# Optimization experiments

Hardware: AMD Instinct MI355X
Metric: run time of the kernel (lower is better)

## Reference

```python
import jax, jax.numpy as jnp
import numpy as np

N, D_IN, D_H, D_OUT, R, E, NB = 50000, 128, 128, 64, 4, 400000, 2

def _xavier(k, shape, fan_in, fan_out):
    # torch xavier_uniform with relu gain sqrt(2)
    lim = np.sqrt(2.0) * np.sqrt(6.0 / (fan_in + fan_out))
    return jax.random.uniform(k, shape, jnp.float32, -lim, lim)

def setup_inputs() -> dict:
    key = jax.random.key(0)
    ks = jax.random.split(key, 9)
    x = jax.random.normal(ks[0], (N, D_IN), dtype=jnp.float32)
    src = jax.random.randint(ks[1], (R, E), 0, N, dtype=jnp.int32)
    dst = jax.random.randint(ks[2], (R, E), 0, N, dtype=jnp.int32)
    inp = {"x": x, "src": src, "dst": dst}
    dims = [(D_IN, D_H), (D_H, D_H), (D_H, D_OUT)]
    for i, (di, do) in enumerate(dims):
        inp[f"basis{i}"] = _xavier(ks[3 + 2 * i], (NB, di, do), di, do)
        inp[f"coeff{i}"] = _xavier(ks[4 + 2 * i], (R, NB), NB, R)
    return inp

def _rel_layer(h, src, dst, basis, coeff):
    """One RelGraphConvLayer: per-relation basis weight + GraphConv(norm='both'),
    summed over relations (HeteroGraphConv aggregate='sum')."""
    n = h.shape[0]
    W = jnp.einsum('rb,bio->rio', coeff, basis)  # [R, d_in, d_out] basis-decomposed weights
    out = jnp.zeros((n, W.shape[-1]), dtype=h.dtype)
    for r in range(src.shape[0]):  # fixed small set of relations
        s, d = src[r], dst[r]
        ones = jnp.ones(s.shape[0], dtype=h.dtype)
        deg_out = jnp.maximum(jax.ops.segment_sum(ones, s, num_segments=n), 1.0)
        deg_in = jnp.maximum(jax.ops.segment_sum(ones, d, num_segments=n), 1.0)
        norm_src = deg_out ** -0.5
        norm_dst = deg_in ** -0.5
        # weight applied before aggregation (d_in >= d_out path of dgl GraphConv; math identical)
        hr = (h * norm_src[:, None]) @ W[r]            # [N, d_out]
        agg = jax.ops.segment_sum(hr[s], d, num_segments=n)  # SpMM via gather + scatter-add
        out = out + agg * norm_dst[:, None]
    return out

def reference(x, src, dst, basis0, coeff0, basis1, coeff1, basis2, coeff2):
    h = jax.nn.relu(_rel_layer(x, src, dst, basis0, coeff0))
    h = jax.nn.relu(_rel_layer(h, src, dst, basis1, coeff1))
    return _rel_layer(h, src, dst, basis2, coeff2)  # final layer: no activation
```

## Files before the change

kernel.cpp:

```cpp
#include <hip/hip_runtime.h>
#include <hip/hip_bf16.h>
#include <cstdint>
#include <cstddef>

#define NN 50000
#define RR 4
#define EE 400000
#define TE (RR*EE)
#define HR 25000
#define RN (RR*NN)
#define NSEG (NN*RR)
#define SCB2 782
#define NBK 512
#define BKSZ 98
#define CHA 4000
#define MAXSPAN 4608

using frag_ab = __attribute__((ext_vector_type(8))) short;
using frag_cd = __attribute__((ext_vector_type(4))) float;

static __device__ __forceinline__ unsigned short f2bf(float f) {
    union { float f; unsigned u; } v; v.f = f;
    unsigned r = (v.u + 0x7FFF + ((v.u >> 16) & 1)) >> 16;
    return (unsigned short)r;
}
static __device__ __forceinline__ unsigned pack2(float lo, float hi) {
    return (unsigned)f2bf(lo) | ((unsigned)f2bf(hi) << 16);
}
static __device__ __forceinline__ float blo(unsigned u) { return __uint_as_float(u << 16); }
static __device__ __forceinline__ float bhi(unsigned u) { return __uint_as_float(u & 0xFFFF0000u); }

__global__ __launch_bounds__(1024) void k_pre(const int* __restrict__ src,
                                              const int* __restrict__ dst,
                                              int* __restrict__ cnt_srcQ,
                                              int* __restrict__ cnt_dstQ,
                                              const float4* __restrict__ x4,
                                              uint2* __restrict__ o,
                                              const float* __restrict__ B0,
                                              const float* __restrict__ B1,
                                              const float* __restrict__ B2,
                                              unsigned short* __restrict__ Bt0,
                                              unsigned short* __restrict__ Bt1,
                                              unsigned short* __restrict__ Bt2) {
    __shared__ unsigned bins[HR / 2];
    int bid = blockIdx.x;
    if (bid < 64) {
        int combo = bid >> 3;
        int range = (bid >> 2) & 1;
        int qc    = bid & 3;
        int r = combo >> 1;
        int side = combo & 1;
        const int* arr = (side == 0 ? src : dst) + (size_t)r * EE + (size_t)qc * (EE / 4);
        int lo = range * HR;
        for (int i = threadIdx.x; i < HR / 2; i += 1024) bins[i] = 0;
        __syncthreads();
        const int4* a4 = (const int4*)arr;
        for (int i = threadIdx.x; i < EE / 16; i += 1024) {
            int4 v = a4[i];
            int t;
            t = v.x - lo; if ((unsigned)t < (unsigned)HR) atomicAdd(&bins[t >> 1], 1u << ((t & 1) * 16));
            t = v.y - lo; if ((unsigned)t < (unsigned)HR) atomicAdd(&bins[t >> 1], 1u << ((t & 1) * 16));
            t = v.z - lo; if ((unsigned)t < (unsigned)HR) atomicAdd(&bins[t >> 1], 1u << ((t & 1) * 16));
            t = v.w - lo; if ((unsigned)t < (unsigned)HR) atomicAdd(&bins[t >> 1], 1u << ((t & 1) * 16));
        }
        __syncthreads();
        int* outp = (side == 0 ? cnt_srcQ : cnt_dstQ) + (size_t)qc * RN + (size_t)r * NN + lo;
        for (int i = threadIdx.x; i < HR / 2; i += 1024) {
            unsigned b = bins[i];
            outp[2 * i]     = (int)(b & 0xFFFFu);
            outp[2 * i + 1] = (int)(b >> 16);
        }
    } else if (bid < 1627) {
        int i = (bid - 64) * 1024 + threadIdx.x;
        if (i < NN * 32) {
            float4 v = x4[i];
            o[i] = make_uint2(pack2(v.x, v.y), pack2(v.z, v.w));
        }
    } else {
        int t = (bid - 1627) * 1024 + threadIdx.x;
        if (t < 32768) {
            int k = t & 255, n = t >> 8;
            Bt0[t] = f2bf(B0[k * 128 + n]);
        } else if (t < 65536) {
            int i = t - 32768;
            int k = i & 255, n = i >> 8;
            Bt1[i] = f2bf(B1[k * 128 + n]);
        } else {
            int i = t - 65536;
            int k = i & 255, n = i >> 8;
            Bt2[i] = f2bf(B2[k * 64 + n]);
        }
    }
}

__global__ __launch_bounds__(256) void k_norms_partial(const int* __restrict__ cnt_srcQ,
                                                       const int* __restrict__ cnt_dstQ,
                                                       float* __restrict__ nsrc,
                                                       float* __restrict__ ndst,
                                                       int* __restrict__ cntd2,
                                                       int* __restrict__ part) {
    __shared__ int s[256];
    int t = threadIdx.x;
    int f = blockIdx.x * 256 + t;
    int v = 0;
    if (f < NSEG) {
        int d = f >> 2, r = f & 3;
        int i = r * NN + d;
        int ss = cnt_srcQ[i] + cnt_srcQ[RN + i] + cnt_srcQ[2 * RN + i] + cnt_srcQ[3 * RN + i];
        int ds = cnt_dstQ[i] + cnt_dstQ[RN + i] + cnt_dstQ[2 * RN + i] + cnt_dstQ[3 * RN + i];
        nsrc[i] = 1.0f / sqrtf(fmaxf((float)ss, 1.0f));
        ndst[i] = 1.0f / sqrtf(fmaxf((float)ds, 1.0f));
        cntd2[f] = ds;
        v = ds;
    }
    s[t] = v;
    __syncthreads();
    for (int off = 128; off > 0; off >>= 1) {
        if (t < off) s[t] += s[t + off];
        __syncthreads();
    }
    if (t == 0) part[blockIdx.x] = s[0];
}

__global__ __launch_bounds__(256) void k_emit2(const int* __restrict__ cntd2,
                                               const int* __restrict__ part,
                                               int* __restrict__ rp2,
                                               int* __restrict__ gcur) {
    __shared__ int red[256];
    __shared__ int s[256];
    int t = threadIdx.x;
    int bid = blockIdx.x;
    int acc = 0;
    for (int j = t; j < bid; j += 256) acc += part[j];
    red[t] = acc;
    __syncthreads();
    for (int off = 128; off > 0; off >>= 1) {
        if (t < off) red[t] += red[t + off];
        __syncthreads();
    }
    int offs0 = red[0];
    __syncthreads();
    int f = bid * 256 + t;
    int v = (f < NSEG) ? cntd2[f] : 0;
    s[t] = v;
    __syncthreads();
    for (int off = 1; off < 256; off <<= 1) {
        int u = (t >= off) ? s[t - off] : 0;
        __syncthreads();
        s[t] += u;
        __syncthreads();
    }
    if (f < NSEG) {
        int rv = offs0 + s[t] - v;
        rp2[f] = rv;
        if (f % (BKSZ * 4) == 0) gcur[f / (BKSZ * 4)] = rv;
    }
    if (f == NSEG - 1) {
        rp2[NSEG] = TE;
        gcur[NBK - 1] = TE;
    }
}

__global__ __launch_bounds__(256) void k_fillA(const int* __restrict__ src,
                                               const int* __restrict__ dst,
                                               int* __restrict__ gcur,
                                               unsigned* __restrict__ stage) {
    __shared__ int cnt[NBK];
    __shared__ int rcur[NBK];
    int r = blockIdx.y;
    int base_e = blockIdx.x * CHA;
    int t = threadIdx.x;
    for (int i = t; i < NBK; i += 256) cnt[i] = 0;
    __syncthreads();
    const int* dr = dst + (size_t)r * EE;
    const int* sr = src + (size_t)r * EE;
    for (int i = base_e + t; i < base_e + CHA; i += 256) {
        int d = dr[i];
        atomicAdd(&cnt[d / BKSZ], 1);
    }
    __syncthreads();
    for (int i = t; i < NBK; i += 256) rcur[i] = atomicAdd(&gcur[i], cnt[i]);
    __syncthreads();
    for (int i = base_e + t; i < base_e + CHA; i += 256) {
        int d = dr[i];
        int s = sr[i];
        int b = d / BKSZ;
        int dl = d - b * BKSZ;
        int pos = atomicAdd(&rcur[b], 1);
        stage[pos] = (unsigned)s | ((unsigned)r << 16) | ((unsigned)dl << 18);
    }
}

__global__ __launch_bounds__(256) void k_fillB(const unsigned* __restrict__ stage,
                                               const int* __restrict__ rp2,
                                               const float* __restrict__ nsrc,
                                               const float* __restrict__ ndst,
                                               uint2* __restrict__ ed) {
    __shared__ unsigned imgU[MAXSPAN];
    __shared__ float imgW[MAXSPAN];
    __shared__ int lcur[BKSZ * 4];
    __shared__ float ndL[BKSZ * 4];
    int b = blockIdx.x;
    int t = threadIdx.x;
    int node0 = b * BKSZ;
    if (node0 >= NN) return;
    int nodes = min(BKSZ, NN - node0);
    int nseg_local = nodes * 4;
    int segbase = node0 * 4;
    for (int i = t; i < nseg_local; i += 256) {
        lcur[i] = rp2[segbase + i];
        ndL[i] = ndst[(i & 3) * NN + node0 + (i >> 2)];
    }
    __syncthreads();
    int S0 = rp2[segbase];
    int S1 = rp2[segbase + nseg_local];
    int span = S1 - S0;
    if (span <= MAXSPAN) {
        for (int i = S0 + t; i < S1; i += 256) {
            unsigned w = stage[i];
            int s = (int)(w & 0xFFFFu);
            int r = (int)((w >> 16) & 3u);
            int dl = (int)(w >> 18);
            int seg = dl * 4 + r;
            int pos = atomicAdd(&lcur[seg], 1);
            int idx = pos - S0;
            imgU[idx] = w & 0x3FFFFu;
            imgW[idx] = nsrc[r * NN + s] * ndL[seg];
        }
        __syncthreads();
        for (int i = t; i < span; i += 256)
            ed[S0 + i] = make_uint2(imgU[i], __float_as_uint(imgW[i]));
    } else {
        for (int i = S0 + t; i < S1; i += 256) {
            unsigned w = stage[i];
            int s = (int)(w & 0xFFFFu);
            int r = (int)((w >> 16) & 3u);
            int dl = (int)(w >> 18);
            int seg = dl * 4 + r;
            int pos = atomicAdd(&lcur[seg], 1);
            ed[pos] = make_uint2(w & 0x3FFFFu,
                                 __float_as_uint(nsrc[r * NN + s] * ndL[seg]));
        }
    }
}

template <int BN, bool BF16OUT>
__global__ __launch_bounds__(256) void k_agg_gemm(const uint4* __restrict__ hb4,
                                                  const int* __restrict__ rp2,
                                                  const uint2* __restrict__ ed,
                                                  const float* __restrict__ coeff,
                                                  const unsigned short* __restrict__ Bt,
                                                  void* __restrict__ Cout) {
    __shared__ uint4 ldsA4[16 * 32];
    char* ldsB = (char*)ldsA4;

    int w = threadIdx.x >> 6;
    int lane = threadIdx.x & 63;
    int q = lane >> 4, hl = lane & 15;
    int node0 = blockIdx.x * 16;

    float c00 = coeff[0], c01 = coeff[1], c10 = coeff[2], c11 = coeff[3];
    float c20 = coeff[4], c21 = coeff[5], c30 = coeff[6], c31 = coeff[7];

#pragma unroll 1
    for (int k4 = 0; k4 < 4; k4++) {
        int rowl = w + k4 * 4;
        int node = node0 + rowl;
        {
            float a00 = 0.f, a01 = 0.f, a02 = 0.f, a03 = 0.f;
            float a04 = 0.f, a05 = 0.f, a06 = 0.f, a07 = 0.f;
            float a10 = 0.f, a11 = 0.f, a12 = 0.f, a13 = 0.f;
            float a14 = 0.f, a15 = 0.f, a16 = 0.f, a17 = 0.f;

            int e0 = rp2[node * 4], e1 = rp2[node * 4 + 4];
            int e = e0;
            uint2 wA = make_uint2(0u, 0u), wB = make_uint2(0u, 0u);
            if (e + 7 < e1) { wA = ed[e + q]; wB = ed[e + 4 + q]; }
            for (; e + 7 < e1; e += 8) {
                uint4 hA = hb4[(size_t)(wA.x & 0xFFFFu) * 16 + hl];
                uint4 hB = hb4[(size_t)(wB.x & 0xFFFFu) * 16 + hl];
                int eN = (e + 15 < e1) ? (e + 8) : e0;
                uint2 nA = ed[eN + q];
                uint2 nB = ed[eN + 4 + q];

                int rA = (int)(wA.x >> 16);
                int rB = (int)(wB.x >> 16);
                float wsA = __uint_as_float(wA.y);
                float wsB = __uint_as_float(wB.y);
                float wa0 = (rA == 0 ? c00 : rA == 1 ? c10 : rA == 2 ? c20 : c30) * wsA;
                float wa1 = (rA == 0 ? c01 : rA == 1 ? c11 : rA == 2 ? c21 : c31) * wsA;
                float wb0 = (rB == 0 ? c00 : rB == 1 ? c10 : rB == 2 ? c20 : c30) * wsB;
                float wb1 = (rB == 0 ? c01 : rB == 1 ? c11 : rB == 2 ? c21 : c31) * wsB;

                float h0 = blo(hA.x), h1 = bhi(hA.x), h2 = blo(hA.y), h3 = bhi(hA.y);
                float h4 = blo(hA.z), h5 = bhi(hA.z), h6 = blo(hA.w), h7 = bhi(hA.w);
                a00 += wa0 * h0; a01 += wa0 * h1; a02 += wa0 * h2; a03 += wa0 * h3;
                a04 += wa0 * h4; a05 += wa0 * h5; a06 += wa0 * h6; a07 += wa0 * h7;
                a10 += wa1 * h0; a11 += wa1 * h1; a12 += wa1 * h2; a13 += wa1 * h3;
                a14 += wa1 * h4; a15 += wa1 * h5; a16 += wa1 * h6; a17 += wa1 * h7;

                h0 = blo(hB.x); h1 = bhi(hB.x); h2 = blo(hB.y); h3 = bhi(hB.y);
                h4 = blo(hB.z); h5 = bhi(hB.z); h6 = blo(hB.w); h7 = bhi(hB.w);
                a00 += wb0 * h0; a01 += wb0 * h1; a02 += wb0 * h2; a03 += wb0 * h3;
                a04 += wb0 * h4; a05 += wb0 * h5; a06 += wb0 * h6; a07 += wb0 * h7;
                a10 += wb1 * h0; a11 += wb1 * h1; a12 += wb1 * h2; a13 += wb1 * h3;
                a14 += wb1 * h4; a15 += wb1 * h5; a16 += wb1 * h6; a17 += wb1 * h7;

                wA = nA; wB = nB;
            }
            for (; e < e1; e += 4) {
                int E = e + q;
                bool act = E < e1;
                uint2 weA = ed[act ? E : e0];
                uint4 hA = hb4[(size_t)(weA.x & 0xFFFFu) * 16 + hl];
                int rA = (int)(weA.x >> 16);
                float wsA = act ? __uint_as_float(weA.y) : 0.f;
                float wa0 = (rA == 0 ? c00 : rA == 1 ? c10 : rA == 2 ? c20 : c30) * wsA;
                float wa1 = (rA == 0 ? c01 : rA == 1 ? c11 : rA == 2 ? c21 : c31) * wsA;
                float h0 = blo(hA.x), h1 = bhi(hA.x), h2 = blo(hA.y), h3 = bhi(hA.y);
                float h4 = blo(hA.z), h5 = bhi(hA.z), h6 = blo(hA.w), h7 = bhi(hA.w);
                a00 += wa0 * h0; a01 += wa0 * h1; a02 += wa0 * h2; a03 += wa0 * h3;
                a04 += wa0 * h4; a05 += wa0 * h5; a06 += wa0 * h6; a07 += wa0 * h7;
                a10 += wa1 * h0; a11 += wa1 * h1; a12 += wa1 * h2; a13 += wa1 * h3;
                a14 += wa1 * h4; a15 += wa1 * h5; a16 += wa1 * h6; a17 += wa1 * h7;
            }

            a00 += __shfl_xor(a00, 16, 64); a00 += __shfl_xor(a00, 32, 64);
            a01 += __shfl_xor(a01, 16, 64); a01 += __shfl_xor(a01, 32, 64);
            a02 += __shfl_xor(a02, 16, 64); a02 += __shfl_xor(a02, 32, 64);
            a03 += __shfl_xor(a03, 16, 64); a03 += __shfl_xor(a03, 32, 64);
            a04 += __shfl_xor(a04, 16, 64); a04 += __shfl_xor(a04, 32, 64);
            a05 += __shfl_xor(a05, 16, 64); a05 += __shfl_xor(a05, 32, 64);
            a06 += __shfl_xor(a06, 16, 64); a06 += __shfl_xor(a06, 32, 64);
            a07 += __shfl_xor(a07, 16, 64); a07 += __shfl_xor(a07, 32, 64);
            a10 += __shfl_xor(a10, 16, 64); a10 += __shfl_xor(a10, 32, 64);
            a11 += __shfl_xor(a11, 16, 64); a11 += __shfl_xor(a11, 32, 64);
            a12 += __shfl_xor(a12, 16, 64); a12 += __shfl_xor(a12, 32, 64);
            a13 += __shfl_xor(a13, 16, 64); a13 += __shfl_xor(a13, 32, 64);
            a14 += __shfl_xor(a14, 16, 64); a14 += __shfl_xor(a14, 32, 64);
            a15 += __shfl_xor(a15, 16, 64); a15 += __shfl_xor(a15, 32, 64);
            a16 += __shfl_xor(a16, 16, 64); a16 += __shfl_xor(a16, 32, 64);
            a17 += __shfl_xor(a17, 16, 64); a17 += __shfl_xor(a17, 32, 64);

            int c = q >> 1, h4 = q & 1;
            float v0 = c ? (h4 ? a14 : a10) : (h4 ? a04 : a00);
            float v1 = c ? (h4 ? a15 : a11) : (h4 ? a05 : a01);
            float v2 = c ? (h4 ? a16 : a12) : (h4 ? a06 : a02);
            float v3 = c ? (h4 ? a17 : a13) : (h4 ? a07 : a03);
            uint2 st;
            st.x = pack2(v0, v1);
            st.y = pack2(v2, v3);
            int idx8 = c * 32 + hl * 2 + h4;
            int boff = rowl * 512 + ((idx8 * 8) ^ ((rowl & 7) << 4));
            *(uint2*)(ldsB + boff) = st;
        }
    }
    __syncthreads();

    int m = lane & 15, qq = lane >> 4;
    constexpr int NTW = BN / 64;

    frag_cd acc[NTW];
#pragma unroll
    for (int t = 0; t < NTW; t++) acc[t] = (frag_cd){0.f, 0.f, 0.f, 0.f};

    int arow = m;
#pragma unroll
    for (int kc = 0; kc < 8; kc++) {
        int aoff = arow * 512 + ((qq * 16 + kc * 64) ^ ((arow & 7) << 4));
        frag_ab a = *(const frag_ab*)(ldsB + aoff);
#pragma unroll
        for (int t = 0; t < NTW; t++) {
            int ct = w * NTW + t;
            frag_ab b = *(const frag_ab*)(Bt + (size_t)(ct * 16 + m) * 256 + kc * 32 + qq * 8);
            acc[t] = __builtin_amdgcn_mfma_f32_16x16x32_bf16(a, b, acc[t], 0, 0, 0);
        }
    }

#pragma unroll
    for (int t = 0; t < NTW; t++) {
#pragma unroll
        for (int i = 0; i < 4; i++) {
            int row = node0 + qq * 4 + i;
            int col = (w * NTW + t) * 16 + m;
            float v = acc[t][i];
            if (BF16OUT) {
                v = fmaxf(v, 0.f);
                ((unsigned short*)Cout)[(size_t)row * BN + col] = f2bf(v);
            } else {
                ((float*)Cout)[(size_t)row * BN + col] = v;
            }
        }
    }
}


extern "C" void kernel_launch(void* const* d_in, const int* in_sizes, int n_in,
                              void* d_out, int out_size, void* d_ws, size_t ws_size,
                              hipStream_t stream) {
    const float* x      = (const float*)d_in[0];
    const int*   src    = (const int*)d_in[1];
    const int*   dst    = (const int*)d_in[2];
    const float* basis0 = (const float*)d_in[3];
    const float* coeff0 = (const float*)d_in[4];
    const float* basis1 = (const float*)d_in[5];
    const float* coeff1 = (const float*)d_in[6];
    const float* basis2 = (const float*)d_in[7];
    const float* coeff2 = (const float*)d_in[8];
    float* out = (float*)d_out;

    char* p = (char*)d_ws;
    auto alloc = [&](size_t bytes) {
        char* r = p;
        p += (bytes + 255) & ~(size_t)255;
        return r;
    };
    int*   cnt_srcQ = (int*)alloc((size_t)4 * RN * 4);
    int*   cnt_dstQ = (int*)alloc((size_t)4 * RN * 4);
    float* nsrc     = (float*)alloc((size_t)RN * 4);
    float* ndst     = (float*)alloc((size_t)RN * 4);
    int*   cntd2    = (int*)alloc((size_t)NSEG * 4);
    int*   rp2      = (int*)alloc((size_t)(NSEG + 1) * 4);
    int*   part     = (int*)alloc((size_t)SCB2 * 4);
    int*   gcur     = (int*)alloc((size_t)NBK * 4);
    unsigned* stage = (unsigned*)alloc((size_t)TE * 4);
    uint2* ed       = (uint2*)alloc((size_t)TE * 8);
    unsigned* Hb    = (unsigned*)alloc((size_t)NN * 64 * 4);
    unsigned* Hb2   = (unsigned*)alloc((size_t)NN * 64 * 4);
    unsigned* Xb    = (unsigned*)alloc((size_t)NN * 64 * 4);
    unsigned short* Bt0 = (unsigned short*)alloc((size_t)128 * 256 * 2);
    unsigned short* Bt1 = (unsigned short*)alloc((size_t)128 * 256 * 2);
    unsigned short* Bt2 = (unsigned short*)alloc((size_t)64 * 256 * 2);

    k_pre<<<1707, 1024, 0, stream>>>(src, dst, cnt_srcQ, cnt_dstQ,
                                     (const float4*)x, (uint2*)Xb,
                                     basis0, basis1, basis2, Bt0, Bt1, Bt2);
    k_norms_partial<<<SCB2, 256, 0, stream>>>(cnt_srcQ, cnt_dstQ, nsrc, ndst, cntd2, part);
    k_emit2<<<SCB2, 256, 0, stream>>>(cntd2, part, rp2, gcur);
    k_fillA<<<dim3(EE / CHA, RR), 256, 0, stream>>>(src, dst, gcur, stage);
    k_fillB<<<NBK, 256, 0, stream>>>(stage, rp2, nsrc, ndst, ed);

    int fusedBlocks = NN / 16;

    k_agg_gemm<128, true><<<fusedBlocks, 256, 0, stream>>>(
        (const uint4*)Xb, rp2, ed, coeff0, Bt0, Hb);
    k_agg_gemm<128, true><<<fusedBlocks, 256, 0, stream>>>(
        (const uint4*)Hb, rp2, ed, coeff1, Bt1, Hb2);
    k_agg_gemm<64, false><<<fusedBlocks, 256, 0, stream>>>(
        (const uint4*)Hb2, rp2, ed, coeff2, Bt2, out);
}
```

Before: 376.9 us.

## Split fused aggregate+GEMM kernel into separate aggregation and MFMA GEMM kernels

Splits the fused kernel, which aggregated 16 nodes per block into LDS and then ran the MFMA GEMM, into two kernels. The aggregation kernel assigns one wave per node and writes a bf16 [N,256] intermediate to global memory, and a separate GEMM kernel reads that intermediate. This removes the __syncthreads barrier and the per-block serial loop of four nodes per wave, so aggregation waves are scheduled freely. In exchange it adds a round trip of the intermediate through global memory and three extra launches. Buffers are also reused: the second layer's output now overwrites Hb, since aggregation finishes before the GEMM writes.

```diff
diff --git a/kernel.cpp b/kernel.cpp
--- a/kernel.cpp
+++ b/kernel.cpp
@@ -244,146 +244,138 @@
     }
 }
 
-template <int BN, bool BF16OUT>
-__global__ __launch_bounds__(256) void k_agg_gemm(const uint4* __restrict__ hb4,
-                                                  const int* __restrict__ rp2,
-                                                  const uint2* __restrict__ ed,
-                                                  const float* __restrict__ coeff,
-                                                  const unsigned short* __restrict__ Bt,
-                                                  void* __restrict__ Cout) {
-    __shared__ uint4 ldsA4[16 * 32];
-    char* ldsB = (char*)ldsA4;
-
-    int w = threadIdx.x >> 6;
+__global__ __launch_bounds__(256) void k_agg(const uint4* __restrict__ hb4,
+                                             const int* __restrict__ rp2,
+                                             const uint2* __restrict__ ed,
+                                             const float* __restrict__ coeff,
+                                             uint2* __restrict__ Mb2) {
+    int wave = (blockIdx.x * 256 + threadIdx.x) >> 6;
     int lane = threadIdx.x & 63;
+    if (wave >= NN) return;
     int q = lane >> 4, hl = lane & 15;
-    int node0 = blockIdx.x * 16;
 
     float c00 = coeff[0], c01 = coeff[1], c10 = coeff[2], c11 = coeff[3];
     float c20 = coeff[4], c21 = coeff[5], c30 = coeff[6], c31 = coeff[7];
 
-#pragma unroll 1
-    for (int k4 = 0; k4 < 4; k4++) {
-        int rowl = w + k4 * 4;
-        int node = node0 + rowl;
-        {
-            float a00 = 0.f, a01 = 0.f, a02 = 0.f, a03 = 0.f;
-            float a04 = 0.f, a05 = 0.f, a06 = 0.f, a07 = 0.f;
-            float a10 = 0.f, a11 = 0.f, a12 = 0.f, a13 = 0.f;
-            float a14 = 0.f, a15 = 0.f, a16 = 0.f, a17 = 0.f;
-
-            int e0 = rp2[node * 4], e1 = rp2[node * 4 + 4];
-            int e = e0;
-            uint2 wA = make_uint2(0u, 0u), wB = make_uint2(0u, 0u);
-            if (e + 7 < e1) { wA = ed[e + q]; wB = ed[e + 4 + q]; }
-            for (; e + 7 < e1; e += 8) {
-                uint4 hA = hb4[(size_t)(wA.x & 0xFFFFu) * 16 + hl];
-                uint4 hB = hb4[(size_t)(wB.x & 0xFFFFu) * 16 + hl];
-                int eN = (e + 15 < e1) ? (e + 8) : e0;
-                uint2 nA = ed[eN + q];
-                uint2 nB = ed[eN + 4 + q];
-
-                int rA = (int)(wA.x >> 16);
-                int rB = (int)(wB.x >> 16);
-                float wsA = __uint_as_float(wA.y);
-                float wsB = __uint_as_float(wB.y);
-                float wa0 = (rA == 0 ? c00 : rA == 1 ? c10 : rA == 2 ? c20 : c30) * wsA;
-                float wa1 = (rA == 0 ? c01 : rA == 1 ? c11 : rA == 2 ? c21 : c31) * wsA;
-                float wb0 = (rB == 0 ? c00 : rB == 1 ? c10 : rB == 2 ? c20 : c30) * wsB;
-                float wb1 = (rB == 0 ? c01 : rB == 1 ? c11 : rB == 2 ? c21 : c31) * wsB;
-
-                float h0 = blo(hA.x), h1 = bhi(hA.x), h2 = blo(hA.y), h3 = bhi(hA.y);
-                float h4 = blo(hA.z), h5 = bhi(hA.z), h6 = blo(hA.w), h7 = bhi(hA.w);
-                a00 += wa0 * h0; a01 += wa0 * h1; a02 += wa0 * h2; a03 += wa0 * h3;
-                a04 += wa0 * h4; a05 += wa0 * h5; a06 += wa0 * h6; a07 += wa0 * h7;
-                a10 += wa1 * h0; a11 += wa1 * h1; a12 += wa1 * h2; a13 += wa1 * h3;
-                a14 += wa1 * h4; a15 += wa1 * h5; a16 += wa1 * h6; a17 += wa1 * h7;
-
-                h0 = blo(hB.x); h1 = bhi(hB.x); h2 = blo(hB.y); h3 = bhi(hB.y);
-                h4 = blo(hB.z); h5 = bhi(hB.z); h6 = blo(hB.w); h7 = bhi(hB.w);
-                a00 += wb0 * h0; a01 += wb0 * h1; a02 += wb0 * h2; a03 += wb0 * h3;
-                a04 += wb0 * h4; a05 += wb0 * h5; a06 += wb0 * h6; a07 += wb0 * h7;
-                a10 += wb1 * h0; a11 += wb1 * h1; a12 += wb1 * h2; a13 += wb1 * h3;
-                a14 += wb1 * h4; a15 += wb1 * h5; a16 += wb1 * h6; a17 += wb1 * h7;
-
-                wA = nA; wB = nB;
-            }
-            for (; e < e1; e += 4) {
-                int E = e + q;
-                bool act = E < e1;
-                uint2 weA = ed[act ? E : e0];
-                uint4 hA = hb4[(size_t)(weA.x & 0xFFFFu) * 16 + hl];
-                int rA = (int)(weA.x >> 16);
-                float wsA = act ? __uint_as_float(weA.y) : 0.f;
-                float wa0 = (rA == 0 ? c00 : rA == 1 ? c10 : rA == 2 ? c20 : c30) * wsA;
-                float wa1 = (rA == 0 ? c01 : rA == 1 ? c11 : rA == 2 ? c21 : c31) * wsA;
-                float h0 = blo(hA.x), h1 = bhi(hA.x), h2 = blo(hA.y), h3 = bhi(hA.y);
-                float h4 = blo(hA.z), h5 = bhi(hA.z), h6 = blo(hA.w), h7 = bhi(hA.w);
-                a00 += wa0 * h0; a01 += wa0 * h1; a02 += wa0 * h2; a03 += wa0 * h3;
-                a04 += wa0 * h4; a05 += wa0 * h5; a06 += wa0 * h6; a07 += wa0 * h7;
-                a10 += wa1 * h0; a11 += wa1 * h1; a12 += wa1 * h2; a13 += wa1 * h3;
-                a14 += wa1 * h4; a15 += wa1 * h5; a16 += wa1 * h6; a17 += wa1 * h7;
-            }
-
-            a00 += __shfl_xor(a00, 16, 64); a00 += __shfl_xor(a00, 32, 64);
-            a01 += __shfl_xor(a01, 16, 64); a01 += __shfl_xor(a01, 32, 64);
-            a02 += __shfl_xor(a02, 16, 64); a02 += __shfl_xor(a02, 32, 64);
-            a03 += __shfl_xor(a03, 16, 64); a03 += __shfl_xor(a03, 32, 64);
-            a04 += __shfl_xor(a04, 16, 64); a04 += __shfl_xor(a04, 32, 64);
-            a05 += __shfl_xor(a05, 16, 64); a05 += __shfl_xor(a05, 32, 64);
-            a06 += __shfl_xor(a06, 16, 64); a06 += __shfl_xor(a06, 32, 64);
-            a07 += __shfl_xor(a07, 16, 64); a07 += __shfl_xor(a07, 32, 64);
-            a10 += __shfl_xor(a10, 16, 64); a10 += __shfl_xor(a10, 32, 64);
-            a11 += __shfl_xor(a11, 16, 64); a11 += __shfl_xor(a11, 32, 64);
-            a12 += __shfl_xor(a12, 16, 64); a12 += __shfl_xor(a12, 32, 64);
-            a13 += __shfl_xor(a13, 16, 64); a13 += __shfl_xor(a13, 32, 64);
-            a14 += __shfl_xor(a14, 16, 64); a14 += __shfl_xor(a14, 32, 64);
-            a15 += __shfl_xor(a15, 16, 64); a15 += __shfl_xor(a15, 32, 64);
-            a16 += __shfl_xor(a16, 16, 64); a16 += __shfl_xor(a16, 32, 64);
-            a17 += __shfl_xor(a17, 16, 64); a17 += __shfl_xor(a17, 32, 64);
-
-            int c = q >> 1, h4 = q & 1;
-            float v0 = c ? (h4 ? a14 : a10) : (h4 ? a04 : a00);
-            float v1 = c ? (h4 ? a15 : a11) : (h4 ? a05 : a01);
-            float v2 = c ? (h4 ? a16 : a12) : (h4 ? a06 : a02);
-            float v3 = c ? (h4 ? a17 : a13) : (h4 ? a07 : a03);
-            uint2 st;
-            st.x = pack2(v0, v1);
-            st.y = pack2(v2, v3);
-            int idx8 = c * 32 + hl * 2 + h4;
-            int boff = rowl * 512 + ((idx8 * 8) ^ ((rowl & 7) << 4));
-            *(uint2*)(ldsB + boff) = st;
-        }
-    }
-    __syncthreads();
-
-    int m = lane & 15, qq = lane >> 4;
-    constexpr int NTW = BN / 64;
-
-    frag_cd acc[NTW];
+    float a00 = 0.f, a01 = 0.f, a02 = 0.f, a03 = 0.f;
+    float a04 = 0.f, a05 = 0.f, a06 = 0.f, a07 = 0.f;
+    float a10 = 0.f, a11 = 0.f, a12 = 0.f, a13 = 0.f;
+    float a14 = 0.f, a15 = 0.f, a16 = 0.f, a17 = 0.f;
+
+    int e0 = rp2[wave * 4], e1 = rp2[wave * 4 + 4];
+
+    int e = e0;
+    uint2 wA = make_uint2(0u, 0u), wB = make_uint2(0u, 0u);
+    if (e + 7 < e1) { wA = ed[e + q]; wB = ed[e + 4 + q]; }
+    for (; e + 7 < e1; e += 8) {
+        uint4 hA = hb4[(size_t)(wA.x & 0xFFFFu) * 16 + hl];
+        uint4 hB = hb4[(size_t)(wB.x & 0xFFFFu) * 16 + hl];
+        int eN = (e + 15 < e1) ? (e + 8) : e0;
+        uint2 nA = ed[eN + q];
+        uint2 nB = ed[eN + 4 + q];
+
+        int rA = (int)(wA.x >> 16);
+        int rB = (int)(wB.x >> 16);
+        float wsA = __uint_as_float(wA.y);
+        float wsB = __uint_as_float(wB.y);
+        float wa0 = (rA == 0 ? c00 : rA == 1 ? c10 : rA == 2 ? c20 : c30) * wsA;
+        float wa1 = (rA == 0 ? c01 : rA == 1 ? c11 : rA == 2 ? c21 : c31) * wsA;
+        float wb0 = (rB == 0 ? c00 : rB == 1 ? c10 : rB == 2 ? c20 : c30) * wsB;
+        float wb1 = (rB == 0 ? c01 : rB == 1 ? c11 : rB == 2 ? c21 : c31) * wsB;
+
+        float h0 = blo(hA.x), h1 = bhi(hA.x), h2 = blo(hA.y), h3 = bhi(hA.y);
+        float h4 = blo(hA.z), h5 = bhi(hA.z), h6 = blo(hA.w), h7 = bhi(hA.w);
+        a00 += wa0 * h0; a01 += wa0 * h1; a02 += wa0 * h2; a03 += wa0 * h3;
+        a04 += wa0 * h4; a05 += wa0 * h5; a06 += wa0 * h6; a07 += wa0 * h7;
+        a10 += wa1 * h0; a11 += wa1 * h1; a12 += wa1 * h2; a13 += wa1 * h3;
+        a14 += wa1 * h4; a15 += wa1 * h5; a16 += wa1 * h6; a17 += wa1 * h7;
+
+        h0 = blo(hB.x); h1 = bhi(hB.x); h2 = blo(hB.y); h3 = bhi(hB.y);
+        h4 = blo(hB.z); h5 = bhi(hB.z); h6 = blo(hB.w); h7 = bhi(hB.w);
+        a00 += wb0 * h0; a01 += wb0 * h1; a02 += wb0 * h2; a03 += wb0 * h3;
+        a04 += wb0 * h4; a05 += wb0 * h5; a06 += wb0 * h6; a07 += wb0 * h7;
+        a10 += wb1 * h0; a11 += wb1 * h1; a12 += wb1 * h2; a13 += wb1 * h3;
+        a14 += wb1 * h4; a15 += wb1 * h5; a16 += wb1 * h6; a17 += wb1 * h7;
+
+        wA = nA; wB = nB;
+    }
+    for (; e < e1; e += 4) {
+        int E = e + q;
+        bool act = E < e1;
+        uint2 weA = ed[act ? E : e0];
+        uint4 hA = hb4[(size_t)(weA.x & 0xFFFFu) * 16 + hl];
+        int rA = (int)(weA.x >> 16);
+        float wsA = act ? __uint_as_float(weA.y) : 0.f;
+        float wa0 = (rA == 0 ? c00 : rA == 1 ? c10 : rA == 2 ? c20 : c30) * wsA;
+        float wa1 = (rA == 0 ? c01 : rA == 1 ? c11 : rA == 2 ? c21 : c31) * wsA;
+        float h0 = blo(hA.x), h1 = bhi(hA.x), h2 = blo(hA.y), h3 = bhi(hA.y);
+        float h4 = blo(hA.z), h5 = bhi(hA.z), h6 = blo(hA.w), h7 = bhi(hA.w);
+        a00 += wa0 * h0; a01 += wa0 * h1; a02 += wa0 * h2; a03 += wa0 * h3;
+        a04 += wa0 * h4; a05 += wa0 * h5; a06 += wa0 * h6; a07 += wa0 * h7;
+        a10 += wa1 * h0; a11 += wa1 * h1; a12 += wa1 * h2; a13 += wa1 * h3;
+        a14 += wa1 * h4; a15 += wa1 * h5; a16 += wa1 * h6; a17 += wa1 * h7;
+    }
+
+    a00 += __shfl_xor(a00, 16, 64); a00 += __shfl_xor(a00, 32, 64);
+    a01 += __shfl_xor(a01, 16, 64); a01 += __shfl_xor(a01, 32, 64);
+    a02 += __shfl_xor(a02, 16, 64); a02 += __shfl_xor(a02, 32, 64);
+    a03 += __shfl_xor(a03, 16, 64); a03 += __shfl_xor(a03, 32, 64);
+    a04 += __shfl_xor(a04, 16, 64); a04 += __shfl_xor(a04, 32, 64);
+    a05 += __shfl_xor(a05, 16, 64); a05 += __shfl_xor(a05, 32, 64);
+    a06 += __shfl_xor(a06, 16, 64); a06 += __shfl_xor(a06, 32, 64);
+    a07 += __shfl_xor(a07, 16, 64); a07 += __shfl_xor(a07, 32, 64);
+    a10 += __shfl_xor(a10, 16, 64); a10 += __shfl_xor(a10, 32, 64);
+    a11 += __shfl_xor(a11, 16, 64); a11 += __shfl_xor(a11, 32, 64);
+    a12 += __shfl_xor(a12, 16, 64); a12 += __shfl_xor(a12, 32, 64);
+    a13 += __shfl_xor(a13, 16, 64); a13 += __shfl_xor(a13, 32, 64);
+    a14 += __shfl_xor(a14, 16, 64); a14 += __shfl_xor(a14, 32, 64);
+    a15 += __shfl_xor(a15, 16, 64); a15 += __shfl_xor(a15, 32, 64);
+    a16 += __shfl_xor(a16, 16, 64); a16 += __shfl_xor(a16, 32, 64);
+    a17 += __shfl_xor(a17, 16, 64); a17 += __shfl_xor(a17, 32, 64);
+
+    int c = q >> 1, h4 = q & 1;
+    float v0 = c ? (h4 ? a14 : a10) : (h4 ? a04 : a00);
+    float v1 = c ? (h4 ? a15 : a11) : (h4 ? a05 : a01);
+    float v2 = c ? (h4 ? a16 : a12) : (h4 ? a06 : a02);
+    float v3 = c ? (h4 ? a17 : a13) : (h4 ? a07 : a03);
+    uint2 st;
+    st.x = pack2(v0, v1);
+    st.y = pack2(v2, v3);
+    Mb2[(size_t)wave * 64 + c * 32 + hl * 2 + h4] = st;
+}
+
+template <int BN, bool BF16OUT>
+__global__ __launch_bounds__(256) void k_gemm(const unsigned short* __restrict__ A,
+                                              const unsigned short* __restrict__ Bt,
+                                              void* __restrict__ Cout) {
+    int wave = threadIdx.x >> 6, lane = threadIdx.x & 63;
+    int row0 = blockIdx.x * 64 + wave * 16;
+    if (row0 >= NN) return;
+    int m = lane & 15, q = lane >> 4;
+    const int NT = BN / 16;
+
+    frag_cd acc[NT];
 #pragma unroll
-    for (int t = 0; t < NTW; t++) acc[t] = (frag_cd){0.f, 0.f, 0.f, 0.f};
-
-    int arow = m;
+    for (int ct = 0; ct < NT; ct++) acc[ct] = (frag_cd){0.f, 0.f, 0.f, 0.f};
+
+    const size_t abase = (size_t)(row0 + m) * 256 + q * 8;
 #pragma unroll
     for (int kc = 0; kc < 8; kc++) {
-        int aoff = arow * 512 + ((qq * 16 + kc * 64) ^ ((arow & 7) << 4));
-        frag_ab a = *(const frag_ab*)(ldsB + aoff);
+        frag_ab a = *(const frag_ab*)(A + abase + kc * 32);
 #pragma unroll
-        for (int t = 0; t < NTW; t++) {
-            int ct = w * NTW + t;
-            frag_ab b = *(const frag_ab*)(Bt + (size_t)(ct * 16 + m) * 256 + kc * 32 + qq * 8);
-            acc[t] = __builtin_amdgcn_mfma_f32_16x16x32_bf16(a, b, acc[t], 0, 0, 0);
+        for (int ct = 0; ct < NT; ct++) {
+            frag_ab b = *(const frag_ab*)(Bt + (size_t)(ct * 16 + m) * 256 + kc * 32 + q * 8);
+            acc[ct] = __builtin_amdgcn_mfma_f32_16x16x32_bf16(a, b, acc[ct], 0, 0, 0);
         }
     }
 
 #pragma unroll
-    for (int t = 0; t < NTW; t++) {
+    for (int ct = 0; ct < NT; ct++) {
 #pragma unroll
         for (int i = 0; i < 4; i++) {
-            int row = node0 + qq * 4 + i;
-            int col = (w * NTW + t) * 16 + m;
-            float v = acc[t][i];
+            int row = row0 + q * 4 + i;
+            int col = ct * 16 + m;
+            float v = acc[ct][i];
             if (BF16OUT) {
                 v = fmaxf(v, 0.f);
                 ((unsigned short*)Cout)[(size_t)row * BN + col] = f2bf(v);
@@ -425,8 +417,8 @@
     int*   gcur     = (int*)alloc((size_t)NBK * 4);
     unsigned* stage = (unsigned*)alloc((size_t)TE * 4);
     uint2* ed       = (uint2*)alloc((size_t)TE * 8);
+    unsigned* Mb    = (unsigned*)alloc((size_t)NN * 128 * 4);
     unsigned* Hb    = (unsigned*)alloc((size_t)NN * 64 * 4);
-    unsigned* Hb2   = (unsigned*)alloc((size_t)NN * 64 * 4);
     unsigned* Xb    = (unsigned*)alloc((size_t)NN * 64 * 4);
     unsigned short* Bt0 = (unsigned short*)alloc((size_t)128 * 256 * 2);
     unsigned short* Bt1 = (unsigned short*)alloc((size_t)128 * 256 * 2);
@@ -440,12 +432,13 @@
     k_fillA<<<dim3(EE / CHA, RR), 256, 0, stream>>>(src, dst, gcur, stage);
     k_fillB<<<NBK, 256, 0, stream>>>(stage, rp2, nsrc, ndst, ed);
 
-    int fusedBlocks = NN / 16;
-
-    k_agg_gemm<128, true><<<fusedBlocks, 256, 0, stream>>>(
-        (const uint4*)Xb, rp2, ed, coeff0, Bt0, Hb);
-    k_agg_gemm<128, true><<<fusedBlocks, 256, 0, stream>>>(
-        (const uint4*)Hb, rp2, ed, coeff1, Bt1, Hb2);
-    k_agg_gemm<64, false><<<fusedBlocks, 256, 0, stream>>>(
-        (const uint4*)Hb2, rp2, ed, coeff2, Bt2, out);
-}
+    int aggBlocks = NN / 4;
+    int gemmBlocks = (NN + 63) / 64;
+
+    k_agg<<<aggBlocks, 256, 0, stream>>>((const uint4*)Xb, rp2, ed, coeff0, (uint2*)Mb);
+    k_gemm<128, true><<<gemmBlocks, 256, 0, stream>>>((const unsigned short*)Mb, Bt0, Hb);
+    k_agg<<<aggBlocks, 256, 0, stream>>>((const uint4*)Hb, rp2, ed, coeff1, (uint2*)Mb);
+    k_gemm<128, true><<<gemmBlocks, 256, 0, stream>>>((const unsigned short*)Mb, Bt1, Hb);
+    k_agg<<<aggBlocks, 256, 0, stream>>>((const uint4*)Hb, rp2, ed, coeff2, (uint2*)Mb);
+    k_gemm<64, false><<<gemmBlocks, 256, 0, stream>>>((const unsigned short*)Mb, Bt2, out);
+}
```

New measurement: 396.4 us. 5.2% more time.
